# Optimization experiments

Measured on AMD Instinct MI355X. Metric: run time of the kernel, lower is better.

## Reference

```python
import jax, jax.numpy as jnp
import numpy as np

L, B, S, D, H, V, F = 4, 2, 2048, 1024, 16, 50257, 4096
DH = D // H

def _ln(x, w, b):
    m = x.mean(-1, keepdims=True)
    v = ((x - m) ** 2).mean(-1, keepdims=True)
    return (x - m) / jnp.sqrt(v + 1e-5) * w + b

def _rope(x):
    # x: [B, H, S, DH]; xformers-style half-split rotation
    dh = x.shape[-1]
    inv = 1.0 / (10000.0 ** (jnp.arange(0, dh, 2, dtype=jnp.float32) / dh))
    t = jnp.arange(x.shape[-2], dtype=jnp.float32)
    fr = t[:, None] * inv[None, :]                      # [S, DH/2]
    emb = jnp.concatenate([fr, fr], axis=-1)            # [S, DH]
    cos, sin = jnp.cos(emb), jnp.sin(emb)
    x1, x2 = jnp.split(x, 2, axis=-1)
    return x * cos + jnp.concatenate([-x2, x1], axis=-1) * sin

def setup_inputs() -> dict:
    key = jax.random.key(0)
    ks = jax.random.split(key, 12)
    d = {}
    d['tokens'] = jax.random.randint(ks[0], (B, S), 0, V)
    d['targets'] = jax.random.randint(ks[1], (B, S), 0, V)
    d['word_emb'] = jax.random.normal(ks[2], (V, D), jnp.float32) * 0.02
    d['pos_emb'] = jax.random.normal(ks[3], (S, D), jnp.float32) * 0.02
    d['ln1_w'] = jnp.ones((L, D), jnp.float32)
    d['ln1_b'] = jnp.zeros((L, D), jnp.float32)
    d['wq'] = jax.random.normal(ks[4], (L, D, D), jnp.float32) * 0.02
    d['bq'] = jnp.zeros((L, D), jnp.float32)
    d['wk'] = jax.random.normal(ks[5], (L, D, D), jnp.float32) * 0.02
    d['bk'] = jnp.zeros((L, D), jnp.float32)
    d['wv'] = jax.random.normal(ks[6], (L, D, D), jnp.float32) * 0.02
    d['bv'] = jnp.zeros((L, D), jnp.float32)
    d['wo'] = jax.random.normal(ks[7], (L, D, D), jnp.float32) * 0.02
    d['bo'] = jnp.zeros((L, D), jnp.float32)
    d['ln2_w'] = jnp.ones((L, D), jnp.float32)
    d['ln2_b'] = jnp.zeros((L, D), jnp.float32)
    d['w1'] = jax.random.normal(ks[8], (L, D, F), jnp.float32) * 0.02
    d['b1'] = jnp.zeros((L, F), jnp.float32)
    d['w2'] = jax.random.normal(ks[9], (L, F, D), jnp.float32) * 0.02
    d['b2'] = jnp.zeros((L, D), jnp.float32)
    d['post_w'] = jnp.ones((D,), jnp.float32)
    d['post_b'] = jnp.zeros((D,), jnp.float32)
    d['lnf_w'] = jnp.ones((D,), jnp.float32)
    d['lnf_b'] = jnp.zeros((D,), jnp.float32)
    d['head_w'] = jax.random.normal(ks[10], (D, V), jnp.float32) * 0.02
    return d

def reference(tokens, targets, word_emb, pos_emb, ln1_w, ln1_b, wq, bq, wk, bk, wv, bv, wo, bo, ln2_w, ln2_b, w1, b1, w2, b2, post_w, post_b, lnf_w, lnf_b, head_w):
    # first encoder's VocabEmbedding: token + learned positional embedding
    x = word_emb[tokens] + pos_emb[None, :S, :]
    mask = jnp.tril(jnp.ones((S, S), dtype=bool))
    scale = 1.0 / float(np.sqrt(DH))
    for i in range(L):
        # pre-norm block-sparse (tril layout == exact causal) attention with RoPE
        h = _ln(x, ln1_w[i], ln1_b[i])
        q = (h @ wq[i] + bq[i]).reshape(B, S, H, DH).transpose(0, 2, 1, 3)
        k = (h @ wk[i] + bk[i]).reshape(B, S, H, DH).transpose(0, 2, 1, 3)
        v = (h @ wv[i] + bv[i]).reshape(B, S, H, DH).transpose(0, 2, 1, 3)
        q, k = _rope(q), _rope(k)
        scores = jnp.einsum('bhqd,bhkd->bhqk', q, k) * scale
        scores = jnp.where(mask, scores, jnp.float32(-1e9))
        att = jax.nn.softmax(scores, axis=-1)
        o = jnp.einsum('bhqk,bhkd->bhqd', att, v).transpose(0, 2, 1, 3).reshape(B, S, D)
        x = x + o @ wo[i] + bo[i]
        # pre-norm MLP
        h2 = _ln(x, ln2_w[i], ln2_b[i])
        x = x + jax.nn.gelu(h2 @ w1[i] + b1[i], approximate=False) @ w2[i] + b2[i]
        if i == L - 1:
            # last encoder block's FF gets an extra Post-norm wrapper
            x = _ln(x, post_w, post_b)
    x = _ln(x, lnf_w, lnf_b)
    logits = x @ head_w                                  # [B, S, V]
    logp = jax.nn.log_softmax(logits, axis=-1)
    nll = -jnp.take_along_axis(logp, targets[..., None], axis=-1)[..., 0]
    return nll.mean()
```

## Files before the change

kernel.cpp:

```cpp
#include <hip/hip_runtime.h>
#include <hip/hip_bf16.h>
#include <math.h>
#include <stdint.h>

constexpr int Lc  = 4;
constexpr int Bc  = 2;
constexpr int Sc  = 2048;
constexpr int Dc  = 1024;
constexpr int Hc  = 16;
constexpr int Vc  = 50257;
constexpr int Fc  = 4096;
constexpr int DHc = 64;
constexpr int Mr  = Bc * Sc;
constexpr int QKVN = 3 * Dc;
constexpr int Vpad = 50304;
constexpr int NVT  = Vpad / 128;
constexpr int NQT  = Sc / 128;
constexpr int NSuperH = (NVT + 7) / 8;

typedef __attribute__((ext_vector_type(8))) short short8;
typedef __attribute__((ext_vector_type(4))) float f32x4;

__device__ __forceinline__ void gl2lds16(const __hip_bfloat16* g, __hip_bfloat16* l) {
    __builtin_amdgcn_global_load_lds(
        (const uint32_t __attribute__((address_space(1)))*)g,
        (uint32_t __attribute__((address_space(3)))*)l, 16, 0, 0);
}

__device__ __forceinline__ void lse_combine(float& m, float& s, float mo, float so) {
    float mn = fmaxf(m, mo);
    s = s * __expf(m - mn) + so * __expf(mo - mn);
    m = mn;
}

__device__ __forceinline__ float fast_gelu(float v) {
    float x  = v * 0.70710678118654752f;
    float ax = fabsf(x);
    float t  = 1.0f / (1.0f + 0.3275911f * ax);
    float y  = t * (0.254829592f + t * (-0.284496736f + t * (1.421413741f +
               t * (-1.453152027f + t * 1.061405429f))));
    float erfv = 1.0f - y * __expf(-ax * ax);
    erfv = (x < 0.f) ? -erfv : erfv;
    return 0.5f * v * (1.0f + erfv);
}

__global__ void embed_kernel(const int* __restrict__ tokens,
                             const float* __restrict__ we,
                             const float* __restrict__ pe,
                             float* __restrict__ x) {
    int row = blockIdx.x;
    int s   = row & (Sc - 1);
    int tok = tokens[row];
    const float* wp = we + (size_t)tok * Dc;
    const float* pp = pe + (size_t)s * Dc;
    float* xp = x + (size_t)row * Dc;
    for (int i = threadIdx.x; i < Dc; i += blockDim.x)
        xp[i] = wp[i] + pp[i];
}

__global__ __launch_bounds__(256) void ln_kernel(const float* __restrict__ x,
                                                 const float* __restrict__ w,
                                                 const float* __restrict__ b,
                                                 float* __restrict__ outF,
                                                 __hip_bfloat16* __restrict__ outB) {
    __shared__ float red[256];
    int row = blockIdx.x;
    int tid = threadIdx.x;
    const float* xp = x + (size_t)row * Dc;
    float s1 = 0.f, s2 = 0.f;
    for (int i = tid; i < Dc; i += 256) {
        float v = xp[i];
        s1 += v; s2 += v * v;
    }
    red[tid] = s1; __syncthreads();
    for (int off = 128; off > 0; off >>= 1) {
        if (tid < off) red[tid] += red[tid + off];
        __syncthreads();
    }
    float mean = red[0] * (1.0f / Dc);
    __syncthreads();
    red[tid] = s2; __syncthreads();
    for (int off = 128; off > 0; off >>= 1) {
        if (tid < off) red[tid] += red[tid + off];
        __syncthreads();
    }
    float var  = red[0] * (1.0f / Dc) - mean * mean;
    float rstd = rsqrtf(var + 1e-5f);
    for (int i = tid; i < Dc; i += 256) {
        float v = (xp[i] - mean) * rstd * w[i] + b[i];
        if (outF) outF[(size_t)row * Dc + i] = v;
        if (outB) outB[(size_t)row * Dc + i] = __float2bfloat16(v);
    }
}

__global__ __launch_bounds__(256) void convw_kernel(const float* __restrict__ W,
                                                    __hip_bfloat16* __restrict__ Wt,
                                                    int K, int srcN) {
    __shared__ float t[32][33];
    int n0 = blockIdx.x * 32, k0 = blockIdx.y * 32;
    int tx = threadIdx.x & 31, ty = threadIdx.x >> 5;
    #pragma unroll
    for (int j = 0; j < 4; j++) {
        int k = k0 + ty + j * 8, n = n0 + tx;
        t[ty + j * 8][tx] = (n < srcN) ? W[(size_t)k * srcN + n] : 0.f;
    }
    __syncthreads();
    #pragma unroll
    for (int j = 0; j < 4; j++) {
        int n = n0 + ty + j * 8, k = k0 + tx;
        Wt[(size_t)n * K + k] = __float2bfloat16(t[tx][ty + j * 8]);
    }
}

__global__ void bcat_kernel(const float* __restrict__ bq, const float* __restrict__ bk,
                            const float* __restrict__ bv, float* __restrict__ o) {
    int i = blockIdx.x * 256 + threadIdx.x;
    if (i < QKVN)
        o[i] = (i < Dc) ? bq[i] : (i < 2 * Dc) ? bk[i - Dc] : bv[i - 2 * Dc];
}

__global__ __launch_bounds__(256) void bgemm_kernel(
    const __hip_bfloat16* __restrict__ A,
    const __hip_bfloat16* __restrict__ Bt,
    const float* __restrict__ bias,
    const float* __restrict__ Cin,
    float* __restrict__ outF,
    __hip_bfloat16* __restrict__ outB,
    int N, int K, int act) {
    __shared__ __align__(16) __hip_bfloat16 As[128 * 32];
    __shared__ __align__(16) __hip_bfloat16 Bs[128 * 32];
    const int tid = threadIdx.x;
    const int bid = blockIdx.x;
    const int sup = bid >> 8, wblk = bid & 255;
    const int rowBase = (wblk & 31) * 128;
    const int colBase = (sup * 8 + (wblk >> 5)) * 128;
    const int w = tid >> 6, lane = tid & 63;
    const int wm = w >> 1, wn = w & 1;
    const int quad = lane >> 4, l16 = lane & 15;

    f32x4 acc[4][4];
    #pragma unroll
    for (int i = 0; i < 4; i++)
        #pragma unroll
        for (int j = 0; j < 4; j++) acc[i][j] = (f32x4){0.f, 0.f, 0.f, 0.f};

    const __hip_bfloat16* a0 = A  + (size_t)(rowBase + (tid >> 2)) * K + (tid & 3) * 8;
    const __hip_bfloat16* b0 = Bt + (size_t)(colBase + (tid >> 2)) * K + (tid & 3) * 8;
    const size_t rstep = (size_t)64 * K;
    __hip_bfloat16* lA = As + tid * 8;
    __hip_bfloat16* lB = Bs + tid * 8;

    for (int k0 = 0; k0 < K; k0 += 32) {
        __syncthreads();
        gl2lds16(a0 + k0,         lA);
        gl2lds16(a0 + k0 + rstep, lA + 2048);
        gl2lds16(b0 + k0,         lB);
        gl2lds16(b0 + k0 + rstep, lB + 2048);
        __syncthreads();

        short8 af[4], bf[4];
        #pragma unroll
        for (int i = 0; i < 4; i++) {
            af[i] = *(const short8*)(As + (wm * 64 + i * 16 + l16) * 32 + quad * 8);
            bf[i] = *(const short8*)(Bs + (wn * 64 + i * 16 + l16) * 32 + quad * 8);
        }
        #pragma unroll
        for (int i = 0; i < 4; i++)
            #pragma unroll
            for (int j = 0; j < 4; j++)
                acc[i][j] = __builtin_amdgcn_mfma_f32_16x16x32_bf16(af[i], bf[j], acc[i][j], 0, 0, 0);
    }

    #pragma unroll
    for (int i = 0; i < 4; i++) {
        #pragma unroll
        for (int j = 0; j < 4; j++) {
            int col = colBase + wn * 64 + j * 16 + l16;
            float bb = bias ? bias[col] : 0.f;
            #pragma unroll
            for (int r = 0; r < 4; r++) {
                int row = rowBase + wm * 64 + i * 16 + quad * 4 + r;
                float v = acc[i][j][r] + bb;
                if (Cin) v += Cin[(size_t)row * N + col];
                if (act) v = fast_gelu(v);
                if (outF) outF[(size_t)row * N + col] = v;
                if (outB) outB[(size_t)row * N + col] = __float2bfloat16(v);
            }
        }
    }
}

__global__ __launch_bounds__(256) void headgemm_kernel(
    const __hip_bfloat16* __restrict__ A,
    const __hip_bfloat16* __restrict__ Bt,
    const int* __restrict__ targets,
    float* __restrict__ pmax, float* __restrict__ psum,
    float* __restrict__ tlog) {
    __shared__ __align__(16) __hip_bfloat16 As[128 * 32];
    __shared__ __align__(16) __hip_bfloat16 Bs[128 * 32];
    __shared__ float pmW[2][128], psW[2][128];
    __shared__ int tg[128];
    const int tid = threadIdx.x;
    const int bid = blockIdx.x;
    const int sup = bid >> 8, wblk = bid & 255;
    const int rowBase = (wblk & 31) * 128;
    const int colT = sup * 8 + (wblk >> 5);
    if (colT >= NVT) return;
    const int colBase = colT * 128;
    const int K = Dc;
    const int w = tid >> 6, lane = tid & 63;
    const int wm = w >> 1, wn = w & 1;
    const int quad = lane >> 4, l16 = lane & 15;

    if (tid < 128) tg[tid] = targets[rowBase + tid];

    f32x4 acc[4][4];
    #pragma unroll
    for (int i = 0; i < 4; i++)
        #pragma unroll
        for (int j = 0; j < 4; j++) acc[i][j] = (f32x4){0.f, 0.f, 0.f, 0.f};

    const __hip_bfloat16* a0 = A  + (size_t)(rowBase + (tid >> 2)) * K + (tid & 3) * 8;
    const __hip_bfloat16* b0 = Bt + (size_t)(colBase + (tid >> 2)) * K + (tid & 3) * 8;
    const size_t rstep = (size_t)64 * K;
    __hip_bfloat16* lA = As + tid * 8;
    __hip_bfloat16* lB = Bs + tid * 8;

    for (int k0 = 0; k0 < K; k0 += 32) {
        __syncthreads();
        gl2lds16(a0 + k0,         lA);
        gl2lds16(a0 + k0 + rstep, lA + 2048);
        gl2lds16(b0 + k0,         lB);
        gl2lds16(b0 + k0 + rstep, lB + 2048);
        __syncthreads();

        short8 af[4], bf[4];
        #pragma unroll
        for (int i = 0; i < 4; i++) {
            af[i] = *(const short8*)(As + (wm * 64 + i * 16 + l16) * 32 + quad * 8);
            bf[i] = *(const short8*)(Bs + (wn * 64 + i * 16 + l16) * 32 + quad * 8);
        }
        #pragma unroll
        for (int i = 0; i < 4; i++)
            #pragma unroll
            for (int j = 0; j < 4; j++)
                acc[i][j] = __builtin_amdgcn_mfma_f32_16x16x32_bf16(af[i], bf[j], acc[i][j], 0, 0, 0);
    }

    #pragma unroll
    for (int i = 0; i < 4; i++) {
        #pragma unroll
        for (int r = 0; r < 4; r++) {
            int rib = wm * 64 + i * 16 + quad * 4 + r;
            int tgt = tg[rib];
            float vals[4];
            float m = -1e30f;
            #pragma unroll
            for (int j = 0; j < 4; j++) {
                int col = colBase + wn * 64 + j * 16 + l16;
                float v = acc[i][j][r];
                bool ok = (col < Vc);
                if (ok && col == tgt) tlog[rowBase + rib] = v;
                vals[j] = ok ? v : -1e30f;
                m = fmaxf(m, vals[j]);
            }
            #pragma unroll
            for (int d = 1; d < 16; d <<= 1)
                m = fmaxf(m, __shfl_xor(m, d, 64));
            float s = 0.f;
            #pragma unroll
            for (int j = 0; j < 4; j++) s += __expf(vals[j] - m);
            #pragma unroll
            for (int d = 1; d < 16; d <<= 1)
                s += __shfl_xor(s, d, 64);
            if (l16 == 0) { pmW[wn][rib] = m; psW[wn][rib] = s; }
        }
    }
    __syncthreads();
    if (tid < 128) {
        float m = pmW[0][tid], s = psW[0][tid];
        lse_combine(m, s, pmW[1][tid], psW[1][tid]);
        pmax[(size_t)colT * Mr + rowBase + tid] = m;
        psum[(size_t)colT * Mr + rowBase + tid] = s;
    }
}

__global__ __launch_bounds__(256) void head_reduce_kernel(
    const float* __restrict__ pmax, const float* __restrict__ psum,
    const float* __restrict__ tlog, float* __restrict__ nll) {
    __shared__ float rm[256], rs[256];
    int row = blockIdx.x;
    int tid = threadIdx.x;
    float m = -1e30f, s = 0.f;
    for (int t = tid; t < NVT; t += 256)
        lse_combine(m, s, pmax[(size_t)t * Mr + row], psum[(size_t)t * Mr + row]);
    rm[tid] = m; rs[tid] = s; __syncthreads();
    for (int off = 128; off > 0; off >>= 1) {
        if (tid < off) {
            float mm = rm[tid], ss = rs[tid];
            lse_combine(mm, ss, rm[tid + off], rs[tid + off]);
            rm[tid] = mm; rs[tid] = ss;
        }
        __syncthreads();
    }
    if (tid == 0) nll[row] = rm[0] + logf(rs[0]) - tlog[row];
}

__global__ void ropecvt_kernel(const __hip_bfloat16* __restrict__ qkvb,
                               __hip_bfloat16* __restrict__ qb,
                               __hip_bfloat16* __restrict__ kb) {
    int p = blockIdx.x * blockDim.x + threadIdx.x;
    if (p >= Mr * Hc * 32) return;
    int j    = p & 31;
    int h    = (p >> 5) & (Hc - 1);
    int srow = p >> 9;
    int s    = srow & (Sc - 1);
    int b    = srow >> 11;
    float inv = powf(10000.0f, -(float)(2 * j) * (1.0f / 64.0f));
    float fr  = (float)s * inv;
    float c = cosf(fr), sn = sinf(fr);
    size_t base = (size_t)srow * QKVN + h * DHc;
    size_t o = ((size_t)(b * Hc + h) * Sc + s) * DHc;
    float q1 = __bfloat162float(qkvb[base + j]);
    float q2 = __bfloat162float(qkvb[base + j + 32]);
    qb[o + j]      = __float2bfloat16((q1 * c - q2 * sn) * 0.125f);
    qb[o + j + 32] = __float2bfloat16((q2 * c + q1 * sn) * 0.125f);
    float k1 = __bfloat162float(qkvb[base + Dc + j]);
    float k2 = __bfloat162float(qkvb[base + Dc + j + 32]);
    kb[o + j]      = __float2bfloat16(k1 * c - k2 * sn);
    kb[o + j + 32] = __float2bfloat16(k2 * c + k1 * sn);
}

__global__ __launch_bounds__(256) void vt_kernel(const __hip_bfloat16* __restrict__ qkvb,
                                                 __hip_bfloat16* __restrict__ vtb) {
    __shared__ float t[32][33];
    int s0 = blockIdx.x * 32, d0 = blockIdx.y * 32;
    int bh = blockIdx.z;
    int b = bh >> 4, h = bh & (Hc - 1);
    int tx = threadIdx.x & 31, ty = threadIdx.x >> 5;
    #pragma unroll
    for (int jj = 0; jj < 4; jj++) {
        int s = s0 + ty + jj * 8;
        t[ty + jj * 8][tx] = __bfloat162float(
            qkvb[((size_t)(b * Sc + s)) * QKVN + 2 * Dc + h * DHc + d0 + tx]);
    }
    __syncthreads();
    #pragma unroll
    for (int jj = 0; jj < 4; jj++) {
        int d = d0 + ty + jj * 8;
        vtb[((size_t)bh * DHc + d) * Sc + s0 + tx] = __float2bfloat16(t[tx][ty + jj * 8]);
    }
}

__global__ __launch_bounds__(256) void attn_mfma_kernel(
    const __hip_bfloat16* __restrict__ qb,
    const __hip_bfloat16* __restrict__ kb,
    const __hip_bfloat16* __restrict__ vtb,
    __hip_bfloat16* __restrict__ ob) {
    __shared__ __align__(16) __hip_bfloat16 Ks[128 * 64];
    __shared__ __align__(16) __hip_bfloat16 Vts[64 * 128];
    __shared__ __align__(16) __hip_bfloat16 Ps[128 * 128];

    const int tid  = threadIdx.x;
    const int idx  = blockIdx.x;
    const int qt   = (NQT - 1) - (idx >> 5);
    const int bh   = idx & 31;
    const int b    = bh >> 4, h = bh & (Hc - 1);
    const int w    = tid >> 6, lane = tid & 63;
    const int quad = lane >> 4, l16 = lane & 15;
    const int sz   = l16 & 7;

    const __hip_bfloat16* kb_bh = kb  + (size_t)bh * Sc * DHc;
    const __hip_bfloat16* vt_bh = vtb + (size_t)bh * DHc * Sc;

    short8 afq[2][2];
    {
        const __hip_bfloat16* qp =
            qb + ((size_t)bh * Sc + qt * 128 + w * 32 + l16) * DHc;
        #pragma unroll
        for (int i = 0; i < 2; i++)
            #pragma unroll
            for (int dc = 0; dc < 2; dc++)
                afq[i][dc] = *(const short8*)(qp + i * 16 * DHc + (dc * 4 + quad) * 8);
    }

    f32x4 oacc[2][4];
    float m[2][4], lsum[2][4];
    #pragma unroll
    for (int i = 0; i < 2; i++)
        #pragma unroll
        for (int dt = 0; dt < 4; dt++) oacc[i][dt] = (f32x4){0.f, 0.f, 0.f, 0.f};
    #pragma unroll
    for (int i = 0; i < 2; i++)
        #pragma unroll
        for (int r = 0; r < 4; r++) { m[i][r] = -1e30f; lsum[i][r] = 0.f; }

    for (int kt = 0; kt <= qt; ++kt) {
        __syncthreads();
        #pragma unroll
        for (int p = 0; p < 4; p++) {
            int k = p * 32 + (tid >> 3);
            gl2lds16(kb_bh + ((size_t)(kt * 128 + k)) * DHc + (((tid & 7) ^ (k & 7)) << 3),
                     Ks + p * 2048 + tid * 8);
        }
        #pragma unroll
        for (int p = 0; p < 4; p++) {
            int d = p * 16 + (tid >> 4);
            gl2lds16(vt_bh + (size_t)d * Sc + kt * 128 + (((tid & 15) ^ (d & 7)) << 3),
                     Vts + p * 2048 + tid * 8);
        }
        __syncthreads();

        f32x4 sacc[2][8];
        #pragma unroll
        for (int i = 0; i < 2; i++)
            #pragma unroll
            for (int j = 0; j < 8; j++) sacc[i][j] = (f32x4){0.f, 0.f, 0.f, 0.f};
        #pragma unroll
        for (int j = 0; j < 8; j++) {
            const __hip_bfloat16* kp = Ks + (j * 16 + l16) * DHc;
            short8 bk0 = *(const short8*)(kp + ((quad ^ sz) << 3));
            short8 bk1 = *(const short8*)(kp + (((4 + quad) ^ sz) << 3));
            #pragma unroll
            for (int i = 0; i < 2; i++) {
                sacc[i][j] = __builtin_amdgcn_mfma_f32_16x16x32_bf16(afq[i][0], bk0, sacc[i][j], 0, 0, 0);
                sacc[i][j] = __builtin_amdgcn_mfma_f32_16x16x32_bf16(afq[i][1], bk1, sacc[i][j], 0, 0, 0);
            }
        }

        const bool diag = (kt == qt);
        #pragma unroll
        for (int i = 0; i < 2; i++) {
            #pragma unroll
            for (int r = 0; r < 4; r++) {
                int rowq = w * 32 + i * 16 + quad * 4 + r;
                float rm = -1e30f;
                #pragma unroll
                for (int j = 0; j < 8; j++) {
                    float v = sacc[i][j][r];
                    if (diag && (j * 16 + l16 > rowq)) v = -1e30f;
                    sacc[i][j][r] = v;
                    rm = fmaxf(rm, v);
                }
                #pragma unroll
                for (int dlt = 1; dlt < 16; dlt <<= 1)
                    rm = fmaxf(rm, __shfl_xor(rm, dlt, 64));
                float mn = fmaxf(m[i][r], rm);
                float fm = __expf(m[i][r] - mn);
                m[i][r] = mn;
                float rs = 0.f;
                #pragma unroll
                for (int j = 0; j < 8; j++) {
                    float pe = __expf(sacc[i][j][r] - mn);
                    sacc[i][j][r] = pe;
                    rs += pe;
                }
                #pragma unroll
                for (int dlt = 1; dlt < 16; dlt <<= 1)
                    rs += __shfl_xor(rs, dlt, 64);
                lsum[i][r] = lsum[i][r] * fm + rs;
                #pragma unroll
                for (int dt = 0; dt < 4; dt++) oacc[i][dt][r] *= fm;
            }
        }

        #pragma unroll
        for (int i = 0; i < 2; i++) {
            #pragma unroll
            for (int r = 0; r < 4; r++) {
                int Q = w * 32 + i * 16 + quad * 4 + r;
                int rowoff = Q * 128;
                int swz = (Q & 7) << 3;
                #pragma unroll
                for (int j = 0; j < 8; j++)
                    Ps[rowoff + ((j * 16 + l16) ^ swz)] = __float2bfloat16(sacc[i][j][r]);
            }
        }

        #pragma unroll
        for (int kc = 0; kc < 4; kc++) {
            int ch = ((kc * 4 + quad) ^ sz) << 3;
            short8 ap[2], bv[4];
            #pragma unroll
            for (int i = 0; i < 2; i++)
                ap[i] = *(const short8*)(Ps + (w * 32 + i * 16 + l16) * 128 + ch);
            #pragma unroll
            for (int dt = 0; dt < 4; dt++)
                bv[dt] = *(const short8*)(Vts + (dt * 16 + l16) * 128 + ch);
            #pragma unroll
            for (int i = 0; i < 2; i++)
                #pragma unroll
                for (int dt = 0; dt < 4; dt++)
                    oacc[i][dt] = __builtin_amdgcn_mfma_f32_16x16x32_bf16(ap[i], bv[dt], oacc[i][dt], 0, 0, 0);
        }
    }

    #pragma unroll
    for (int i = 0; i < 2; i++) {
        #pragma unroll
        for (int r = 0; r < 4; r++) {
            float inv = 1.0f / lsum[i][r];
            int s = qt * 128 + w * 32 + i * 16 + quad * 4 + r;
            size_t base = ((size_t)b * Sc + s) * Dc + h * DHc;
            #pragma unroll
            for (int dt = 0; dt < 4; dt++)
                ob[base + dt * 16 + l16] = __float2bfloat16(oacc[i][dt][r] * inv);
        }
    }
}

__global__ __launch_bounds__(256) void loss_kernel(const float* __restrict__ nll,
                                                   float* __restrict__ out) {
    __shared__ float red[256];
    int tid = threadIdx.x;
    float s = 0.f;
    for (int i = tid; i < Mr; i += 256) s += nll[i];
    red[tid] = s; __syncthreads();
    for (int off = 128; off > 0; off >>= 1) {
        if (tid < off) red[tid] += red[tid + off];
        __syncthreads();
    }
    if (tid == 0) out[0] = red[0] * (1.0f / Mr);
}

extern "C" void kernel_launch(void* const* d_in, const int* in_sizes, int n_in,
                              void* d_out, int out_size, void* d_ws, size_t ws_size,
                              hipStream_t stream) {
    const int*   tokens   = (const int*)  d_in[0];
    const int*   targets  = (const int*)  d_in[1];
    const float* word_emb = (const float*)d_in[2];
    const float* pos_emb  = (const float*)d_in[3];
    const float* ln1_w    = (const float*)d_in[4];
    const float* ln1_b    = (const float*)d_in[5];
    const float* wq       = (const float*)d_in[6];
    const float* bq       = (const float*)d_in[7];
    const float* wk       = (const float*)d_in[8];
    const float* bk       = (const float*)d_in[9];
    const float* wv       = (const float*)d_in[10];
    const float* bv       = (const float*)d_in[11];
    const float* wo       = (const float*)d_in[12];
    const float* bo       = (const float*)d_in[13];
    const float* ln2_w    = (const float*)d_in[14];
    const float* ln2_b    = (const float*)d_in[15];
    const float* w1       = (const float*)d_in[16];
    const float* b1       = (const float*)d_in[17];
    const float* w2       = (const float*)d_in[18];
    const float* b2       = (const float*)d_in[19];
    const float* post_w   = (const float*)d_in[20];
    const float* post_b   = (const float*)d_in[21];
    const float* lnf_w    = (const float*)d_in[22];
    const float* lnf_b    = (const float*)d_in[23];
    const float* head_w   = (const float*)d_in[24];

    float* cur = (float*)d_ws;
    float* x    = cur; cur += (size_t)Mr * Dc;
    float* nll  = cur; cur += Mr;
    float* tlog = cur; cur += Mr;
    float* bqkv = cur; cur += QKVN;
    float* pmax = cur; cur += (size_t)NVT * Mr;
    float* psum = cur; cur += (size_t)NVT * Mr;
    __hip_bfloat16* bcur = (__hip_bfloat16*)cur;
    __hip_bfloat16* hb     = bcur; bcur += (size_t)Mr * Dc;
    __hip_bfloat16* ob     = bcur; bcur += (size_t)Mr * Dc;
    __hip_bfloat16* midb   = bcur; bcur += (size_t)Mr * Fc;
    __hip_bfloat16* qkvb   = bcur; bcur += (size_t)Mr * QKVN;
    __hip_bfloat16* qb     = bcur; bcur += (size_t)Mr * Dc;
    __hip_bfloat16* kbuf   = bcur; bcur += (size_t)Mr * Dc;
    __hip_bfloat16* Wqkv_t = bcur; bcur += (size_t)QKVN * Dc;
    __hip_bfloat16* Wo_t   = bcur; bcur += (size_t)Dc * Dc;
    __hip_bfloat16* W1_t   = bcur; bcur += (size_t)Fc * Dc;
    __hip_bfloat16* W2_t   = bcur; bcur += (size_t)Dc * Fc;
    __hip_bfloat16* Wh_t   = bcur; bcur += (size_t)Vpad * Dc;
    __hip_bfloat16* vtb = midb;

    dim3 blk(256);

    embed_kernel<<<Mr, blk, 0, stream>>>(tokens, word_emb, pos_emb, x);
    convw_kernel<<<dim3(Vpad / 32, Dc / 32), blk, 0, stream>>>(head_w, Wh_t, Dc, Vc);

    for (int l = 0; l < Lc; l++) {
        convw_kernel<<<dim3(Dc / 32, Dc / 32), blk, 0, stream>>>(wq + (size_t)l * Dc * Dc, Wqkv_t, Dc, Dc);
        convw_kernel<<<dim3(Dc / 32, Dc / 32), blk, 0, stream>>>(wk + (size_t)l * Dc * Dc, Wqkv_t + (size_t)Dc * Dc, Dc, Dc);
        convw_kernel<<<dim3(Dc / 32, Dc / 32), blk, 0, stream>>>(wv + (size_t)l * Dc * Dc, Wqkv_t + (size_t)2 * Dc * Dc, Dc, Dc);
        bcat_kernel<<<QKVN / 256, blk, 0, stream>>>(bq + l * Dc, bk + l * Dc, bv + l * Dc, bqkv);

        ln_kernel<<<Mr, blk, 0, stream>>>(x, ln1_w + l * Dc, ln1_b + l * Dc, nullptr, hb);
        bgemm_kernel<<<(QKVN / 1024) * 256, blk, 0, stream>>>(
            hb, Wqkv_t, bqkv, nullptr, nullptr, qkvb, QKVN, Dc, 0);
        ropecvt_kernel<<<(Mr * Hc * 32) / 256, blk, 0, stream>>>(qkvb, qb, kbuf);
        vt_kernel<<<dim3(Sc / 32, DHc / 32, Bc * Hc), blk, 0, stream>>>(qkvb, vtb);
        attn_mfma_kernel<<<Bc * Hc * NQT, blk, 0, stream>>>(qb, kbuf, vtb, ob);

        convw_kernel<<<dim3(Dc / 32, Dc / 32), blk, 0, stream>>>(wo + (size_t)l * Dc * Dc, Wo_t, Dc, Dc);
        bgemm_kernel<<<(Dc / 1024) * 256, blk, 0, stream>>>(
            ob, Wo_t, bo + l * Dc, x, x, nullptr, Dc, Dc, 0);

        ln_kernel<<<Mr, blk, 0, stream>>>(x, ln2_w + l * Dc, ln2_b + l * Dc, nullptr, hb);
        convw_kernel<<<dim3(Fc / 32, Dc / 32), blk, 0, stream>>>(w1 + (size_t)l * Dc * Fc, W1_t, Dc, Fc);
        bgemm_kernel<<<(Fc / 1024) * 256, blk, 0, stream>>>(
            hb, W1_t, b1 + l * Fc, nullptr, nullptr, midb, Fc, Dc, 1);
        convw_kernel<<<dim3(Dc / 32, Fc / 32), blk, 0, stream>>>(w2 + (size_t)l * Fc * Dc, W2_t, Fc, Dc);
        bgemm_kernel<<<(Dc / 1024) * 256, blk, 0, stream>>>(
            midb, W2_t, b2 + l * Dc, x, x, nullptr, Dc, Fc, 0);

        if (l == Lc - 1)
            ln_kernel<<<Mr, blk, 0, stream>>>(x, post_w, post_b, x, nullptr);
    }

    ln_kernel<<<Mr, blk, 0, stream>>>(x, lnf_w, lnf_b, nullptr, hb);
    headgemm_kernel<<<NSuperH * 256, blk, 0, stream>>>(hb, Wh_t, targets, pmax, psum, tlog);
    head_reduce_kernel<<<Mr, blk, 0, stream>>>(pmax, psum, tlog, nll);
    loss_kernel<<<1, blk, 0, stream>>>(nll, (float*)d_out);
}
```

Measured before the change: 2.974 ms.

## Add 256x256 double-buffered swizzled GEMM for QKV, FFN1 and LM head

```diff
diff --git a/kernel.cpp b/kernel.cpp
--- a/kernel.cpp
+++ b/kernel.cpp
@@ -13,10 +13,9 @@
 constexpr int DHc = 64;
 constexpr int Mr  = Bc * Sc;
 constexpr int QKVN = 3 * Dc;
-constexpr int Vpad = 50304;
-constexpr int NVT  = Vpad / 128;
+constexpr int Vpad = 50432;
+constexpr int NVT  = Vpad / 256;
 constexpr int NQT  = Sc / 128;
-constexpr int NSuperH = (NVT + 7) / 8;
 
 typedef __attribute__((ext_vector_type(8))) short short8;
 typedef __attribute__((ext_vector_type(4))) float f32x4;
@@ -190,86 +189,197 @@
     }
 }
 
-__global__ __launch_bounds__(256) void headgemm_kernel(
+__global__ __launch_bounds__(512, 2) void bgemm256_kernel(
+    const __hip_bfloat16* __restrict__ A,
+    const __hip_bfloat16* __restrict__ Bt,
+    const float* __restrict__ bias,
+    const float* __restrict__ Cin,
+    float* __restrict__ outF,
+    __hip_bfloat16* __restrict__ outB,
+    int N, int K, int act, int NCT) {
+    __shared__ __align__(16) __hip_bfloat16 As[2][256 * 64];
+    __shared__ __align__(16) __hip_bfloat16 Bs[2][256 * 64];
+    const int tid = threadIdx.x;
+    const int bid = blockIdx.x;
+    const int sup = bid >> 6, wblk = bid & 63;
+    const int colT = sup * 4 + (wblk >> 4);
+    if (colT >= NCT) return;
+    const int rowBase = (wblk & 15) * 256;
+    const int colBase = colT * 256;
+    const int w = tid >> 6, lane = tid & 63;
+    const int wm = w >> 2, wn = w & 3;
+    const int quad = lane >> 4, l16 = lane & 15;
+
+    f32x4 acc[8][4];
+    #pragma unroll
+    for (int i = 0; i < 8; i++)
+        #pragma unroll
+        for (int n = 0; n < 4; n++) acc[i][n] = (f32x4){0.f, 0.f, 0.f, 0.f};
+
+    const int srow = tid >> 3;
+    const int swz  = (tid & 7) ^ (srow & 7);
+    const __hip_bfloat16* aS = A  + (size_t)(rowBase + srow) * K + swz * 8;
+    const __hip_bfloat16* bS = Bt + (size_t)(colBase + srow) * K + swz * 8;
+    const size_t jstep = (size_t)64 * K;
+
+    const int nt = K >> 6;
+    #pragma unroll
+    for (int j = 0; j < 4; j++) gl2lds16(aS + j * jstep, &As[0][j * 4096 + tid * 8]);
+    #pragma unroll
+    for (int j = 0; j < 4; j++) gl2lds16(bS + j * jstep, &Bs[0][j * 4096 + tid * 8]);
+    __syncthreads();
+
+    for (int t = 0; t < nt; t++) {
+        if (t + 1 < nt) {
+            const int nb = (t + 1) & 1;
+            const int k0 = (t + 1) << 6;
+            #pragma unroll
+            for (int j = 0; j < 4; j++) gl2lds16(aS + j * jstep + k0, &As[nb][j * 4096 + tid * 8]);
+            #pragma unroll
+            for (int j = 0; j < 4; j++) gl2lds16(bS + j * jstep + k0, &Bs[nb][j * 4096 + tid * 8]);
+        }
+        const __hip_bfloat16* as = As[t & 1];
+        const __hip_bfloat16* bs = Bs[t & 1];
+        #pragma unroll
+        for (int ks = 0; ks < 2; ks++) {
+            short8 bf[4], af[8];
+            #pragma unroll
+            for (int n = 0; n < 4; n++) {
+                int row = wn * 64 + n * 16 + l16;
+                bf[n] = *(const short8*)(bs + row * 64 + (((ks * 4 + quad) ^ (row & 7)) << 3));
+            }
+            #pragma unroll
+            for (int i = 0; i < 8; i++) {
+                int row = wm * 128 + i * 16 + l16;
+                af[i] = *(const short8*)(as + row * 64 + (((ks * 4 + quad) ^ (row & 7)) << 3));
+            }
+            #pragma unroll
+            for (int i = 0; i < 8; i++)
+                #pragma unroll
+                for (int n = 0; n < 4; n++)
+                    acc[i][n] = __builtin_amdgcn_mfma_f32_16x16x32_bf16(af[i], bf[n], acc[i][n], 0, 0, 0);
+        }
+        __syncthreads();
+    }
+
+    #pragma unroll
+    for (int i = 0; i < 8; i++) {
+        #pragma unroll
+        for (int n = 0; n < 4; n++) {
+            int col = colBase + wn * 64 + n * 16 + l16;
+            float bb = bias ? bias[col] : 0.f;
+            #pragma unroll
+            for (int r = 0; r < 4; r++) {
+                int row = rowBase + wm * 128 + i * 16 + quad * 4 + r;
+                float v = acc[i][n][r] + bb;
+                if (Cin) v += Cin[(size_t)row * N + col];
+                if (act) v = fast_gelu(v);
+                if (outF) outF[(size_t)row * N + col] = v;
+                if (outB) outB[(size_t)row * N + col] = __float2bfloat16(v);
+            }
+        }
+    }
+}
+
+__global__ __launch_bounds__(512, 2) void headgemm256_kernel(
     const __hip_bfloat16* __restrict__ A,
     const __hip_bfloat16* __restrict__ Bt,
     const int* __restrict__ targets,
     float* __restrict__ pmax, float* __restrict__ psum,
     float* __restrict__ tlog) {
-    __shared__ __align__(16) __hip_bfloat16 As[128 * 32];
-    __shared__ __align__(16) __hip_bfloat16 Bs[128 * 32];
-    __shared__ float pmW[2][128], psW[2][128];
-    __shared__ int tg[128];
+    __shared__ __align__(16) __hip_bfloat16 As[2][256 * 64];
+    __shared__ __align__(16) __hip_bfloat16 Bs[2][256 * 64];
+    __shared__ float pmW[4][256], psW[4][256];
+    __shared__ int tg[256];
     const int tid = threadIdx.x;
     const int bid = blockIdx.x;
-    const int sup = bid >> 8, wblk = bid & 255;
-    const int rowBase = (wblk & 31) * 128;
-    const int colT = sup * 8 + (wblk >> 5);
+    const int sup = bid >> 6, wblk = bid & 63;
+    const int colT = sup * 4 + (wblk >> 4);
     if (colT >= NVT) return;
-    const int colBase = colT * 128;
+    const int rowBase = (wblk & 15) * 256;
+    const int colBase = colT * 256;
     const int K = Dc;
     const int w = tid >> 6, lane = tid & 63;
-    const int wm = w >> 1, wn = w & 1;
+    const int wm = w >> 2, wn = w & 3;
     const int quad = lane >> 4, l16 = lane & 15;
 
-    if (tid < 128) tg[tid] = targets[rowBase + tid];
-
-    f32x4 acc[4][4];
-    #pragma unroll
-    for (int i = 0; i < 4; i++)
-        #pragma unroll
-        for (int j = 0; j < 4; j++) acc[i][j] = (f32x4){0.f, 0.f, 0.f, 0.f};
-
-    const __hip_bfloat16* a0 = A  + (size_t)(rowBase + (tid >> 2)) * K + (tid & 3) * 8;
-    const __hip_bfloat16* b0 = Bt + (size_t)(colBase + (tid >> 2)) * K + (tid & 3) * 8;
-    const size_t rstep = (size_t)64 * K;
-    __hip_bfloat16* lA = As + tid * 8;
-    __hip_bfloat16* lB = Bs + tid * 8;
-
-    for (int k0 = 0; k0 < K; k0 += 32) {
-        __syncthreads();
-        gl2lds16(a0 + k0,         lA);
-        gl2lds16(a0 + k0 + rstep, lA + 2048);
-        gl2lds16(b0 + k0,         lB);
-        gl2lds16(b0 + k0 + rstep, lB + 2048);
-        __syncthreads();
-
-        short8 af[4], bf[4];
-        #pragma unroll
-        for (int i = 0; i < 4; i++) {
-            af[i] = *(const short8*)(As + (wm * 64 + i * 16 + l16) * 32 + quad * 8);
-            bf[i] = *(const short8*)(Bs + (wn * 64 + i * 16 + l16) * 32 + quad * 8);
-        }
-        #pragma unroll
-        for (int i = 0; i < 4; i++)
-            #pragma unroll
-            for (int j = 0; j < 4; j++)
-                acc[i][j] = __builtin_amdgcn_mfma_f32_16x16x32_bf16(af[i], bf[j], acc[i][j], 0, 0, 0);
-    }
-
-    #pragma unroll
-    for (int i = 0; i < 4; i++) {
+    if (tid < 256) tg[tid] = targets[rowBase + tid];
+
+    f32x4 acc[8][4];
+    #pragma unroll
+    for (int i = 0; i < 8; i++)
+        #pragma unroll
+        for (int n = 0; n < 4; n++) acc[i][n] = (f32x4){0.f, 0.f, 0.f, 0.f};
+
+    const int srow = tid >> 3;
+    const int swz  = (tid & 7) ^ (srow & 7);
+    const __hip_bfloat16* aS = A  + (size_t)(rowBase + srow) * K + swz * 8;
+    const __hip_bfloat16* bS = Bt + (size_t)(colBase + srow) * K + swz * 8;
+    const size_t jstep = (size_t)64 * K;
+
+    const int nt = K >> 6;
+    #pragma unroll
+    for (int j = 0; j < 4; j++) gl2lds16(aS + j * jstep, &As[0][j * 4096 + tid * 8]);
+    #pragma unroll
+    for (int j = 0; j < 4; j++) gl2lds16(bS + j * jstep, &Bs[0][j * 4096 + tid * 8]);
+    __syncthreads();
+
+    for (int t = 0; t < nt; t++) {
+        if (t + 1 < nt) {
+            const int nb = (t + 1) & 1;
+            const int k0 = (t + 1) << 6;
+            #pragma unroll
+            for (int j = 0; j < 4; j++) gl2lds16(aS + j * jstep + k0, &As[nb][j * 4096 + tid * 8]);
+            #pragma unroll
+            for (int j = 0; j < 4; j++) gl2lds16(bS + j * jstep + k0, &Bs[nb][j * 4096 + tid * 8]);
+        }
+        const __hip_bfloat16* as = As[t & 1];
+        const __hip_bfloat16* bs = Bs[t & 1];
+        #pragma unroll
+        for (int ks = 0; ks < 2; ks++) {
+            short8 bf[4], af[8];
+            #pragma unroll
+            for (int n = 0; n < 4; n++) {
+                int row = wn * 64 + n * 16 + l16;
+                bf[n] = *(const short8*)(bs + row * 64 + (((ks * 4 + quad) ^ (row & 7)) << 3));
+            }
+            #pragma unroll
+            for (int i = 0; i < 8; i++) {
+                int row = wm * 128 + i * 16 + l16;
+                af[i] = *(const short8*)(as + row * 64 + (((ks * 4 + quad) ^ (row & 7)) << 3));
+            }
+            #pragma unroll
+            for (int i = 0; i < 8; i++)
+                #pragma unroll
+                for (int n = 0; n < 4; n++)
+                    acc[i][n] = __builtin_amdgcn_mfma_f32_16x16x32_bf16(af[i], bf[n], acc[i][n], 0, 0, 0);
+        }
+        __syncthreads();
+    }
+
+    #pragma unroll
+    for (int i = 0; i < 8; i++) {
         #pragma unroll
         for (int r = 0; r < 4; r++) {
-            int rib = wm * 64 + i * 16 + quad * 4 + r;
+            int rib = wm * 128 + i * 16 + quad * 4 + r;
             int tgt = tg[rib];
             float vals[4];
             float m = -1e30f;
             #pragma unroll
-            for (int j = 0; j < 4; j++) {
-                int col = colBase + wn * 64 + j * 16 + l16;
-                float v = acc[i][j][r];
+            for (int n = 0; n < 4; n++) {
+                int col = colBase + wn * 64 + n * 16 + l16;
+                float v = acc[i][n][r];
                 bool ok = (col < Vc);
                 if (ok && col == tgt) tlog[rowBase + rib] = v;
-                vals[j] = ok ? v : -1e30f;
-                m = fmaxf(m, vals[j]);
+                vals[n] = ok ? v : -1e30f;
+                m = fmaxf(m, vals[n]);
             }
             #pragma unroll
             for (int d = 1; d < 16; d <<= 1)
                 m = fmaxf(m, __shfl_xor(m, d, 64));
             float s = 0.f;
             #pragma unroll
-            for (int j = 0; j < 4; j++) s += __expf(vals[j] - m);
+            for (int n = 0; n < 4; n++) s += __expf(vals[n] - m);
             #pragma unroll
             for (int d = 1; d < 16; d <<= 1)
                 s += __shfl_xor(s, d, 64);
@@ -277,9 +387,11 @@
         }
     }
     __syncthreads();
-    if (tid < 128) {
+    if (tid < 256) {
         float m = pmW[0][tid], s = psW[0][tid];
         lse_combine(m, s, pmW[1][tid], psW[1][tid]);
+        lse_combine(m, s, pmW[2][tid], psW[2][tid]);
+        lse_combine(m, s, pmW[3][tid], psW[3][tid]);
         pmax[(size_t)colT * Mr + rowBase + tid] = m;
         psum[(size_t)colT * Mr + rowBase + tid] = s;
     }
@@ -574,6 +686,7 @@
     __hip_bfloat16* vtb = midb;
 
     dim3 blk(256);
+    dim3 blk512(512);
 
     embed_kernel<<<Mr, blk, 0, stream>>>(tokens, word_emb, pos_emb, x);
     convw_kernel<<<dim3(Vpad / 32, Dc / 32), blk, 0, stream>>>(head_w, Wh_t, Dc, Vc);
@@ -585,8 +698,8 @@
         bcat_kernel<<<QKVN / 256, blk, 0, stream>>>(bq + l * Dc, bk + l * Dc, bv + l * Dc, bqkv);
 
         ln_kernel<<<Mr, blk, 0, stream>>>(x, ln1_w + l * Dc, ln1_b + l * Dc, nullptr, hb);
-        bgemm_kernel<<<(QKVN / 1024) * 256, blk, 0, stream>>>(
-            hb, Wqkv_t, bqkv, nullptr, nullptr, qkvb, QKVN, Dc, 0);
+        bgemm256_kernel<<<(QKVN / 1024) * 64, blk512, 0, stream>>>(
+            hb, Wqkv_t, bqkv, nullptr, nullptr, qkvb, QKVN, Dc, 0, QKVN / 256);
         ropecvt_kernel<<<(Mr * Hc * 32) / 256, blk, 0, stream>>>(qkvb, qb, kbuf);
         vt_kernel<<<dim3(Sc / 32, DHc / 32, Bc * Hc), blk, 0, stream>>>(qkvb, vtb);
         attn_mfma_kernel<<<Bc * Hc * NQT, blk, 0, stream>>>(qb, kbuf, vtb, ob);
@@ -597,8 +710,8 @@
 
         ln_kernel<<<Mr, blk, 0, stream>>>(x, ln2_w + l * Dc, ln2_b + l * Dc, nullptr, hb);
         convw_kernel<<<dim3(Fc / 32, Dc / 32), blk, 0, stream>>>(w1 + (size_t)l * Dc * Fc, W1_t, Dc, Fc);
-        bgemm_kernel<<<(Fc / 1024) * 256, blk, 0, stream>>>(
-            hb, W1_t, b1 + l * Fc, nullptr, nullptr, midb, Fc, Dc, 1);
+        bgemm256_kernel<<<(Fc / 1024) * 64, blk512, 0, stream>>>(
+            hb, W1_t, b1 + l * Fc, nullptr, nullptr, midb, Fc, Dc, 1, Fc / 256);
         convw_kernel<<<dim3(Dc / 32, Fc / 32), blk, 0, stream>>>(w2 + (size_t)l * Fc * Dc, W2_t, Fc, Dc);
         bgemm_kernel<<<(Dc / 1024) * 256, blk, 0, stream>>>(
             midb, W2_t, b2 + l * Dc, x, x, nullptr, Dc, Fc, 0);
@@ -608,7 +721,8 @@
     }
 
     ln_kernel<<<Mr, blk, 0, stream>>>(x, lnf_w, lnf_b, nullptr, hb);
-    headgemm_kernel<<<NSuperH * 256, blk, 0, stream>>>(hb, Wh_t, targets, pmax, psum, tlog);
+    headgemm256_kernel<<<((NVT + 3) / 4) * 64, blk512, 0, stream>>>(
+        hb, Wh_t, targets, pmax, psum, tlog);
     head_reduce_kernel<<<Mr, blk, 0, stream>>>(pmax, psum, tlog, nll);
     loss_kernel<<<1, blk, 0, stream>>>(nll, (float*)d_out);
 }
```

Measured after the change: 2.827 ms. -4.9%, faster.
